# Optimization experiments

Measured on AMD Instinct MI355X. Metric: run time of the kernel, lower is better.

Reference implementation:

```python
import jax, jax.numpy as jnp
import numpy as np

B, S, HID = 2, 2048, 2048
NH, NKV, D = 32, 4, 64
N_REP = NH // NKV
EPS = 1e-6
ROPE_THETA = 10000.0


def _rotate_half(x):
    h = x.shape[-1] // 2
    return jnp.concatenate([-x[..., h:], x[..., :h]], axis=-1)


def _rmsnorm(x, gamma):
    # RMSNorm over last dim (head_dim)
    return x * jax.lax.rsqrt(jnp.mean(x * x, axis=-1, keepdims=True) + EPS) * gamma


def setup_inputs() -> dict:
    key = jax.random.key(0)
    ks = jax.random.split(key, 8)
    hidden_states = jax.random.normal(ks[0], (B, S, HID), dtype=jnp.float32)
    # rotary cos/sin tables, shape [B, S, D]
    pos = jnp.arange(S, dtype=jnp.float32)
    inv_freq = 1.0 / (ROPE_THETA ** (jnp.arange(0, D, 2, dtype=jnp.float32) / D))
    freqs = pos[:, None] * inv_freq[None, :]            # [S, D/2]
    emb = jnp.concatenate([freqs, freqs], axis=-1)      # [S, D]
    cos = jnp.broadcast_to(jnp.cos(emb)[None], (B, S, D))
    sin = jnp.broadcast_to(jnp.sin(emb)[None], (B, S, D))
    sc = 0.02
    Wq = jax.random.normal(ks[1], (NH * D, HID), dtype=jnp.float32) * sc
    Wk = jax.random.normal(ks[2], (NKV * D, HID), dtype=jnp.float32) * sc
    Wv = jax.random.normal(ks[3], (NKV * D, HID), dtype=jnp.float32) * sc
    Wg = jax.random.normal(ks[4], (NH * D, HID), dtype=jnp.float32) * sc
    Wo = jax.random.normal(ks[5], (HID, NH * D), dtype=jnp.float32) * sc
    q_gamma = jnp.ones((D,), dtype=jnp.float32)
    k_gamma = jnp.ones((D,), dtype=jnp.float32)
    return dict(hidden_states=hidden_states, cos=cos, sin=sin,
                Wq=Wq, Wk=Wk, Wv=Wv, Wg=Wg, Wo=Wo,
                q_gamma=q_gamma, k_gamma=k_gamma)


def reference(hidden_states, cos, sin, Wq, Wk, Wv, Wg, Wo, q_gamma, k_gamma):
    b, s, _ = hidden_states.shape
    q = (hidden_states @ Wq.T).reshape(b, s, NH, D)
    k = (hidden_states @ Wk.T).reshape(b, s, NKV, D)
    v = (hidden_states @ Wv.T).reshape(b, s, NKV, D)
    gate = hidden_states @ Wg.T                       # [B, S, NH*D]
    # per-head RMSNorm on q/k
    q = _rmsnorm(q, q_gamma)
    k = _rmsnorm(k, k_gamma)
    # [B, H, S, D]
    q = q.transpose(0, 2, 1, 3)
    k = k.transpose(0, 2, 1, 3)
    v = v.transpose(0, 2, 1, 3)
    # RoPE (unsqueeze_dim=1)
    c = cos[:, None, :, :]
    sn = sin[:, None, :, :]
    q = q * c + _rotate_half(q) * sn
    k = k * c + _rotate_half(k) * sn
    # GQA: repeat kv heads
    kr = jnp.repeat(k, N_REP, axis=1)
    vr = jnp.repeat(v, N_REP, axis=1)
    scaling = D ** -0.5
    scores = jnp.einsum('bhqd,bhkd->bhqk', q, kr) * scaling
    w = jax.nn.softmax(scores.astype(jnp.float32), axis=-1).astype(q.dtype)
    out = jnp.einsum('bhqk,bhkd->bhqd', w, vr)
    out = out.transpose(0, 2, 1, 3).reshape(b, s, NH * D)
    out = out * jax.nn.sigmoid(gate)
    return out @ Wo.T
```

## Files before the change

### kernel.cpp

```cpp
#include <hip/hip_runtime.h>


#define LOG2E 1.44269504088896340736f

typedef __attribute__((ext_vector_type(4))) float f32x4;
typedef __attribute__((ext_vector_type(8))) short bf16x8;

__device__ __forceinline__ float bf2f(unsigned short u) {
  union { unsigned u; float f; } x; x.u = ((unsigned)u) << 16; return x.f;
}
__device__ __forceinline__ unsigned short f2bf(float f) {
  union { float f; unsigned u; } x; x.f = f;
  unsigned r = x.u + 0x7fffu + ((x.u >> 16) & 1u);
  return (unsigned short)(r >> 16);
}

__device__ __forceinline__ void async16(void* lds, const void* g) {
  __builtin_amdgcn_global_load_lds(
      (const __attribute__((address_space(1))) unsigned*)g,
      (__attribute__((address_space(3))) unsigned*)lds, 16, 0, 0);
}
__device__ __forceinline__ void lds_fence() {
  __asm__ volatile("s_waitcnt lgkmcnt(0)" ::: "memory");
}

__global__ __launch_bounds__(256) void cvt_all(
    const float* __restrict__ s0, const float* __restrict__ s1,
    const float* __restrict__ s2, const float* __restrict__ s3,
    const float* __restrict__ s4, const float* __restrict__ s5,
    unsigned short* __restrict__ d0, unsigned short* __restrict__ d1,
    unsigned short* __restrict__ d2, unsigned short* __restrict__ d3,
    unsigned short* __restrict__ d4, unsigned short* __restrict__ d5) {
  const long total = 5505024;
  const long stride = (long)gridDim.x * 256;
  for (long i = (long)blockIdx.x * 256 + threadIdx.x; i < total; i += stride) {
    const float* s; unsigned short* d; long off;
    if      (i < 2097152) { s = s0; d = d0; off = 0; }
    else if (i < 3145728) { s = s1; d = d1; off = 2097152; }
    else if (i < 3276800) { s = s2; d = d2; off = 3145728; }
    else if (i < 3407872) { s = s3; d = d3; off = 3276800; }
    else if (i < 4456448) { s = s4; d = d4; off = 3407872; }
    else                  { s = s5; d = d5; off = 4456448; }
    long j = i - off;
    float4 v = reinterpret_cast<const float4*>(s)[j];
    ushort4 u;
    u.x = f2bf(v.x); u.y = f2bf(v.y); u.z = f2bf(v.z); u.w = f2bf(v.w);
    reinterpret_cast<ushort4*>(d)[j] = u;
  }
}

__device__ __forceinline__ void gemm_main_big(
    const unsigned short* __restrict__ A, const unsigned short* __restrict__ W,
    int m0, int n0, unsigned short* lds, f32x4 acc[4][4]) {
  const int tid = threadIdx.x;
  const int w = tid >> 6, l = tid & 63, quad = l >> 4, l16 = l & 15;
  const int wm = (w & 1) * 64, wn = (w >> 1) * 64;
  const int rlo = tid >> 2, ch = tid & 3;

  const f32x4 Z4 = {0.f, 0.f, 0.f, 0.f};
#pragma unroll
  for (int i = 0; i < 4; i++)
#pragma unroll
    for (int j = 0; j < 4; j++) acc[i][j] = Z4;

  const unsigned short* gA =
      A + (size_t)(m0 + rlo) * 2048 + ((ch ^ ((rlo >> 1) & 3)) * 8);
  const unsigned short* gB =
      W + (size_t)(n0 + rlo) * 2048 + ((ch ^ ((rlo >> 1) & 3)) * 8);

  int arow[4], brow[4];
#pragma unroll
  for (int mt = 0; mt < 4; mt++) arow[mt] = (wm + mt * 16 + l16) * 32;
#pragma unroll
  for (int nt = 0; nt < 4; nt++) brow[nt] = (wn + nt * 16 + l16) * 32;
  const int fx = (quad ^ ((l16 >> 1) & 3)) * 8;

  unsigned short* const bA = lds;
  unsigned short* const bB = lds + 12288;

#pragma unroll
  for (int tt = 0; tt < 2; ++tt) {
    const int ko = tt * 32;
    async16(bA + tt * 4096 + tid * 8,        gA + ko);
    async16(bB + tt * 8192 + tid * 8,        gB + ko);
    async16(bB + tt * 8192 + 4096 + tid * 8, gB + 262144 + ko);
  }
  __asm__ volatile("s_waitcnt vmcnt(3)" ::: "memory");
  __builtin_amdgcn_s_barrier();

  int cb = 0;
  for (int t = 0; t < 64; ++t) {
    unsigned short* cA = bA + cb * 4096;
    unsigned short* cB = bB + cb * 8192;

    if (t < 62) {
      int nb = cb + 2; if (nb >= 3) nb -= 3;
      const int ko = (t + 2) * 32;
      async16(bA + nb * 4096 + tid * 8,        gA + ko);
      async16(bB + nb * 8192 + tid * 8,        gB + ko);
      async16(bB + nb * 8192 + 4096 + tid * 8, gB + 262144 + ko);
    }
    bf16x8 af[4], bf[4];
#pragma unroll
    for (int mt = 0; mt < 4; mt++)
      af[mt] = *(const bf16x8*)&cA[arow[mt] + fx];
#pragma unroll
    for (int nt = 0; nt < 4; nt++)
      bf[nt] = *(const bf16x8*)&cB[brow[nt] + fx];
    __builtin_amdgcn_s_barrier();
    __asm__ volatile("s_waitcnt lgkmcnt(0)" ::: "memory");
    __builtin_amdgcn_sched_barrier(0);
    __builtin_amdgcn_s_setprio(1);
#pragma unroll
    for (int mt = 0; mt < 4; mt++)
#pragma unroll
      for (int nt = 0; nt < 4; nt++)
        acc[mt][nt] = __builtin_amdgcn_mfma_f32_16x16x32_bf16(
            af[mt], bf[nt], acc[mt][nt], 0, 0, 0);
    __builtin_amdgcn_s_setprio(0);
    if (t < 62) {
      __asm__ volatile("s_waitcnt vmcnt(3)" ::: "memory");
    } else if (t == 62) {
      __asm__ volatile("s_waitcnt vmcnt(0)" ::: "memory");
    }
    __builtin_amdgcn_s_barrier();
    cb++; if (cb == 3) cb = 0;
  }
}

__global__ __launch_bounds__(512, 4) void gemm_qkvg(
    const unsigned short* __restrict__ X,
    const unsigned short* __restrict__ Wq, const unsigned short* __restrict__ Wk,
    const unsigned short* __restrict__ Wv, const unsigned short* __restrict__ Wg,
    const float* __restrict__ cosb, const float* __restrict__ sinb,
    const float* __restrict__ qg, const float* __restrict__ kg,
    unsigned short* __restrict__ Qn, unsigned short* __restrict__ Kn,
    unsigned short* __restrict__ Vt, unsigned short* __restrict__ gate) {
  __shared__ __attribute__((aligned(16))) unsigned short lds[36864];
  const int ny = blockIdx.y;
  const unsigned short* W; int n0, type;
  if (ny < 8)       { W = Wq; n0 = ny * 256;        type = 0; }
  else if (ny == 8) { W = Wk; n0 = 0;               type = 1; }
  else if (ny == 9) { W = Wv; n0 = 0;               type = 2; }
  else              { W = Wg; n0 = (ny - 10) * 256; type = 3; }
  const int m0 = blockIdx.x * 128;

  f32x4 acc[4][4];
  gemm_main_big(X, W, m0, n0, lds, acc);

  const int tid = threadIdx.x;
  const int w = tid >> 6, l = tid & 63, quad = l >> 4, l16 = l & 15;
  const int wm = (w & 1) * 64, wn = (w >> 1) * 64;

  if (type == 3) {
#pragma unroll
    for (int mt = 0; mt < 4; mt++)
#pragma unroll
      for (int r = 0; r < 4; r++) {
        int row = m0 + wm + mt * 16 + quad * 4 + r;
#pragma unroll
        for (int nt = 0; nt < 4; nt++)
          gate[(size_t)row * 2048 + n0 + wn + nt * 16 + l16] =
              f2bf(acc[mt][nt][r]);
      }
    return;
  }
  if (type == 2) {
#pragma unroll
    for (int mt = 0; mt < 4; mt++)
#pragma unroll
      for (int r = 0; r < 4; r++) {
        int row = m0 + wm + mt * 16 + quad * 4 + r;
        int b = row >> 11, s = row & 2047;
#pragma unroll
        for (int nt = 0; nt < 4; nt++) {
          int col = wn + nt * 16 + l16;
          int kvh = col >> 6, d = col & 63;
          Vt[((size_t)(b * 4 + kvh) * 64 + d) * 2048 + s] =
              f2bf(acc[mt][nt][r]);
        }
      }
    return;
  }

  const float* gamma = (type == 0) ? qg : kg;
  const float scale  = (type == 0) ? 0.125f : LOG2E;
  const int hb = (n0 + wn) >> 6;
  float gv[4];
#pragma unroll
  for (int nt = 0; nt < 4; nt++) gv[nt] = gamma[nt * 16 + l16];

#pragma unroll
  for (int mt = 0; mt < 4; mt++)
#pragma unroll
    for (int r = 0; r < 4; r++) {
      int row = m0 + wm + mt * 16 + quad * 4 + r;
      float ss = 0.f;
#pragma unroll
      for (int nt = 0; nt < 4; nt++) {
        float v = acc[mt][nt][r]; ss += v * v;
      }
#pragma unroll
      for (int off = 1; off < 16; off <<= 1) ss += __shfl_xor(ss, off);
      float rr = rsqrtf(ss * (1.0f / 64.0f) + 1e-6f);
      float xn[4];
#pragma unroll
      for (int nt = 0; nt < 4; nt++) xn[nt] = acc[mt][nt][r] * rr * gv[nt];
      int b = row >> 11, s = row & 2047;
      unsigned short* dst = (type == 0)
          ? Qn + ((size_t)(b * 32 + hb) * 2048 + s) * 64
          : Kn + ((size_t)(b * 4 + hb) * 2048 + s) * 64;
#pragma unroll
      for (int nt = 0; nt < 4; nt++) {
        int d = nt * 16 + l16;
        float rot = (nt < 2) ? -xn[nt ^ 2] : xn[nt ^ 2];
        float cv = cosb[(size_t)row * 64 + d];
        float sv = sinb[(size_t)row * 64 + d];
        dst[d] = f2bf((xn[nt] * cv + rot * sv) * scale);
      }
    }
}

__global__ __launch_bounds__(512, 2) void gemm_out_k(
    const unsigned short* __restrict__ A, const unsigned short* __restrict__ W,
    float* __restrict__ C) {
  __shared__ __attribute__((aligned(16))) unsigned short lds[65536];
  const int m0 = blockIdx.x * 128, n0 = blockIdx.y * 256;
  f32x4 acc[4][4];
  gemm_main_big(A, W, m0, n0, lds, acc);
  const int tid = threadIdx.x;
  const int w = tid >> 6, l = tid & 63, quad = l >> 4, l16 = l & 15;
  const int wm = (w & 1) * 64, wn = (w >> 1) * 64;
#pragma unroll
  for (int mt = 0; mt < 4; mt++)
#pragma unroll
    for (int nt = 0; nt < 4; nt++) {
      int row = m0 + wm + mt * 16 + quad * 4;
      int col = n0 + wn + nt * 16 + l16;
#pragma unroll
      for (int r = 0; r < 4; r++)
        C[(size_t)(row + r) * 2048 + col] = acc[mt][nt][r];
    }
}

__global__ __launch_bounds__(256, 4) void attn(
    const unsigned short* __restrict__ Qn, const unsigned short* __restrict__ Kn,
    const unsigned short* __restrict__ Vt, const unsigned short* __restrict__ gate,
    unsigned short* __restrict__ act) {
  __shared__ __attribute__((aligned(16))) unsigned short smem[20480];
  unsigned short* Ps = smem + 16384;

  const int tid = threadIdx.x, w = tid >> 6, l = tid & 63;
  const int quad = l >> 4, l16 = l & 15, l7 = l16 & 7;
  const int bh = blockIdx.y, b = bh >> 5, h = bh & 31, kvh = h >> 3;
  const int q0 = blockIdx.x * 128;

  const unsigned short* Qg = Qn + ((size_t)(b * 32 + h) * 2048 + q0) * 64;
  const unsigned short* Kg = Kn + (size_t)(b * 4 + kvh) * 2048 * 64;
  const unsigned short* Vg = Vt + (size_t)(b * 4 + kvh) * 64 * 2048;
  unsigned short* Pw = Ps + w * 1024;

  const int kq_src = ((tid & 7) ^ ((tid >> 3) & 7)) * 8;

#pragma unroll
  for (int i = 0; i < 4; i++)
    async16(smem + i * 2048 + tid * 8,
            Qg + (size_t)(i * 32 + (tid >> 3)) * 64 + kq_src);
  __syncthreads();
  bf16x8 qf[2][2];
#pragma unroll
  for (int mt = 0; mt < 2; mt++)
#pragma unroll
    for (int ks = 0; ks < 2; ks++) {
      int row = w * 32 + mt * 16 + l16;
      qf[mt][ks] = *(const bf16x8*)&smem[row * 64 + ((ks * 4 + quad) ^ l7) * 8];
    }
  __syncthreads();

  const f32x4 Z4 = {0.f, 0.f, 0.f, 0.f};
  f32x4 O[2][4];
  float lp[2][4];
#pragma unroll
  for (int mt = 0; mt < 2; mt++) {
#pragma unroll
    for (int nt = 0; nt < 4; nt++) O[mt][nt] = Z4;
#pragma unroll
    for (int r = 0; r < 4; r++) lp[mt][r] = 0.f;
  }

#pragma unroll
  for (int i = 0; i < 2; i++) {
    async16(smem + i * 2048 + tid * 8,
            Kg + (size_t)(i * 32 + (tid >> 3)) * 64 + kq_src);
    async16(smem + 4096 + i * 2048 + tid * 8,
            Vg + (size_t)(i * 32 + (tid >> 3)) * 2048 + kq_src);
  }

  for (int kt = 0; kt < 32; kt++) {
    __syncthreads();

    if (kt < 31) {
      unsigned short* nb = smem + ((kt + 1) & 1) * 8192;
      const int s1 = (kt + 1) * 64;
#pragma unroll
      for (int i = 0; i < 2; i++) {
        async16(nb + i * 2048 + tid * 8,
                Kg + (size_t)(s1 + i * 32 + (tid >> 3)) * 64 + kq_src);
        async16(nb + 4096 + i * 2048 + tid * 8,
                Vg + (size_t)(i * 32 + (tid >> 3)) * 2048 + s1 + kq_src);
      }
    }

    unsigned short* Ks  = smem + (kt & 1) * 8192;
    unsigned short* Vts = Ks + 4096;

    f32x4 sc[2][4];
#pragma unroll
    for (int mt = 0; mt < 2; mt++)
#pragma unroll
      for (int nt = 0; nt < 4; nt++) sc[mt][nt] = Z4;
    __builtin_amdgcn_s_setprio(1);
#pragma unroll
    for (int nt = 0; nt < 4; nt++) {
      int row = nt * 16 + l16;
      bf16x8 kf0 = *(const bf16x8*)&Ks[row * 64 + (quad ^ l7) * 8];
      bf16x8 kf1 = *(const bf16x8*)&Ks[row * 64 + ((4 + quad) ^ l7) * 8];
#pragma unroll
      for (int mt = 0; mt < 2; mt++) {
        sc[mt][nt] = __builtin_amdgcn_mfma_f32_16x16x32_bf16(qf[mt][0], kf0, sc[mt][nt], 0, 0, 0);
        sc[mt][nt] = __builtin_amdgcn_mfma_f32_16x16x32_bf16(qf[mt][1], kf1, sc[mt][nt], 0, 0, 0);
      }
    }
    __builtin_amdgcn_s_setprio(0);

#pragma unroll
    for (int ks2 = 0; ks2 < 2; ks2++) {
#pragma unroll
      for (int mt = 0; mt < 2; mt++)
#pragma unroll
        for (int ntl = 0; ntl < 2; ntl++) {
          int nt = ks2 * 2 + ntl;
#pragma unroll
          for (int r = 0; r < 4; r++) {
            float p = __builtin_amdgcn_exp2f(sc[mt][nt][r]);
            union { float f; unsigned u; } x; x.f = p;
            union { unsigned u; float f; } t; t.u = x.u & 0xffff0000u;
            lp[mt][r] += t.f;
            int q = mt * 16 + quad * 4 + r;
            int c = ntl * 2 + (l16 >> 3);
            int phys = c ^ ((q >> 1) & 3);
            Pw[q * 32 + phys * 8 + l7] = (unsigned short)(x.u >> 16);
          }
        }
      lds_fence();

      bf16x8 pf[2];
#pragma unroll
      for (int mt = 0; mt < 2; mt++) {
        int q = mt * 16 + l16;
        int phys = quad ^ ((l16 >> 1) & 3);
        pf[mt] = *(const bf16x8*)&Pw[q * 32 + phys * 8];
      }
      __builtin_amdgcn_s_setprio(1);
#pragma unroll
      for (int nt2 = 0; nt2 < 4; nt2++) {
        int d = nt2 * 16 + l16;
        bf16x8 vf = *(const bf16x8*)&Vts[d * 64 + ((ks2 * 4 + quad) ^ l7) * 8];
#pragma unroll
        for (int mt = 0; mt < 2; mt++)
          O[mt][nt2] = __builtin_amdgcn_mfma_f32_16x16x32_bf16(
              pf[mt], vf, O[mt][nt2], 0, 0, 0);
      }
      __builtin_amdgcn_s_setprio(0);
      lds_fence();
    }
  }

#pragma unroll
  for (int mt = 0; mt < 2; mt++)
#pragma unroll
    for (int r = 0; r < 4; r++) {
      float s = lp[mt][r];
#pragma unroll
      for (int off = 1; off < 16; off <<= 1) s += __shfl_xor(s, off);
      lp[mt][r] = s;
    }

#pragma unroll
  for (int mt = 0; mt < 2; mt++) {
    float inv[4];
#pragma unroll
    for (int r = 0; r < 4; r++) inv[r] = 1.0f / lp[mt][r];
#pragma unroll
    for (int nt = 0; nt < 4; nt++)
#pragma unroll
      for (int r = 0; r < 4; r++) {
        int srow = q0 + w * 32 + mt * 16 + quad * 4 + r;
        int col = h * 64 + nt * 16 + l16;
        size_t off = (size_t)(b * 2048 + srow) * 2048 + col;
        float g = bf2f(gate[off]);
        float sig = 1.0f / (1.0f + __builtin_amdgcn_exp2f(-g * LOG2E));
        act[off] = f2bf(O[mt][nt][r] * inv[r] * sig);
      }
  }
}

extern "C" void kernel_launch(void* const* d_in, const int* in_sizes, int n_in,
                              void* d_out, int out_size, void* d_ws, size_t ws_size,
                              hipStream_t stream) {
  const float* hid  = (const float*)d_in[0];
  const float* cosb = (const float*)d_in[1];
  const float* sinb = (const float*)d_in[2];
  const float* Wq   = (const float*)d_in[3];
  const float* Wk   = (const float*)d_in[4];
  const float* Wv   = (const float*)d_in[5];
  const float* Wg   = (const float*)d_in[6];
  const float* Wo   = (const float*)d_in[7];
  const float* qg   = (const float*)d_in[8];
  const float* kg   = (const float*)d_in[9];
  float* out = (float*)d_out;

  char* ws = (char*)d_ws;
  unsigned short* Xb   = (unsigned short*)(ws);
  unsigned short* WqB  = (unsigned short*)(ws + 16777216);
  unsigned short* WkB  = (unsigned short*)(ws + 25165824);
  unsigned short* WvB  = (unsigned short*)(ws + 26214400);
  unsigned short* WgB  = (unsigned short*)(ws + 27262976);
  unsigned short* WoB  = (unsigned short*)(ws + 35651584);
  unsigned short* gate = (unsigned short*)(ws + 44040192);
  unsigned short* Qn   = (unsigned short*)(ws + 60817408);
  unsigned short* Kn   = (unsigned short*)(ws + 77594624);
  unsigned short* Vt   = (unsigned short*)(ws + 79691776);
  unsigned short* act = WqB;

  cvt_all<<<dim3(2048), dim3(256), 0, stream>>>(
      hid, Wq, Wk, Wv, Wg, Wo, Xb, WqB, WkB, WvB, WgB, WoB);

  gemm_qkvg<<<dim3(32, 18), dim3(512), 0, stream>>>(
      Xb, WqB, WkB, WvB, WgB, cosb, sinb, qg, kg, Qn, Kn, Vt, gate);

  attn<<<dim3(16, 64), dim3(256), 0, stream>>>(Qn, Kn, Vt, gate, act);

  gemm_out_k<<<dim3(32, 8), dim3(512), 0, stream>>>(act, WoB, out);
}
```

Measured before the change: 382.7 us.

## Shrink QKVG GEMM tile to 128x128 with 256-thread blocks

Replaces the 128x256-tile, 512-thread QKVG projection GEMM with a 128x128-tile, 256-thread variant that uses a three-stage async LDS pipeline and a smaller shared buffer. The grid doubles to 36 column blocks, and the Vt epilogue now adds the column offset. The aim is more blocks to balance load across CUs and higher occupancy from the reduced LDS footprint. In exchange, each block reuses loaded data less, so global and LDS traffic per FLOP goes up.

```diff
diff --git a/kernel.cpp b/kernel.cpp
--- a/kernel.cpp
+++ b/kernel.cpp
@@ -49,6 +49,87 @@
   }
 }
 
+__device__ __forceinline__ void gemm_core128(
+    const unsigned short* __restrict__ A, const unsigned short* __restrict__ W,
+    int m0, int n0, unsigned short* lds, f32x4 acc[4][4]) {
+  const int tid = threadIdx.x;
+  const int w = tid >> 6, l = tid & 63, quad = l >> 4, l16 = l & 15;
+  const int wm = (w & 1) * 64, wn = (w >> 1) * 64;
+  const int rlo = tid >> 2, ch = tid & 3;
+
+  const f32x4 Z4 = {0.f, 0.f, 0.f, 0.f};
+#pragma unroll
+  for (int i = 0; i < 4; i++)
+#pragma unroll
+    for (int j = 0; j < 4; j++) acc[i][j] = Z4;
+
+  const unsigned short* gA =
+      A + (size_t)(m0 + rlo) * 2048 + ((ch ^ ((rlo >> 1) & 3)) * 8);
+  const unsigned short* gB =
+      W + (size_t)(n0 + rlo) * 2048 + ((ch ^ ((rlo >> 1) & 3)) * 8);
+
+  int arow[4], brow[4];
+#pragma unroll
+  for (int mt = 0; mt < 4; mt++) arow[mt] = (wm + mt * 16 + l16) * 32;
+#pragma unroll
+  for (int nt = 0; nt < 4; nt++) brow[nt] = (wn + nt * 16 + l16) * 32;
+  const int fx = (quad ^ ((l16 >> 1) & 3)) * 8;
+
+  unsigned short* const bA = lds;
+  unsigned short* const bB = lds + 12288;
+
+#pragma unroll
+  for (int tt = 0; tt < 2; ++tt) {
+    const int ko = tt * 32;
+    async16(bA + tt * 4096 + tid * 8,        gA + ko);
+    async16(bA + tt * 4096 + 2048 + tid * 8, gA + 131072 + ko);
+    async16(bB + tt * 4096 + tid * 8,        gB + ko);
+    async16(bB + tt * 4096 + 2048 + tid * 8, gB + 131072 + ko);
+  }
+  __asm__ volatile("s_waitcnt vmcnt(4)" ::: "memory");
+  __builtin_amdgcn_s_barrier();
+
+  int cb = 0;
+  for (int t = 0; t < 64; ++t) {
+    unsigned short* cA = bA + cb * 4096;
+    unsigned short* cB = bB + cb * 4096;
+
+    if (t < 62) {
+      int nb = cb + 2; if (nb >= 3) nb -= 3;
+      const int ko = (t + 2) * 32;
+      async16(bA + nb * 4096 + tid * 8,        gA + ko);
+      async16(bA + nb * 4096 + 2048 + tid * 8, gA + 131072 + ko);
+      async16(bB + nb * 4096 + tid * 8,        gB + ko);
+      async16(bB + nb * 4096 + 2048 + tid * 8, gB + 131072 + ko);
+    }
+    bf16x8 af[4], bf[4];
+#pragma unroll
+    for (int mt = 0; mt < 4; mt++)
+      af[mt] = *(const bf16x8*)&cA[arow[mt] + fx];
+#pragma unroll
+    for (int nt = 0; nt < 4; nt++)
+      bf[nt] = *(const bf16x8*)&cB[brow[nt] + fx];
+    __builtin_amdgcn_s_barrier();
+    __asm__ volatile("s_waitcnt lgkmcnt(0)" ::: "memory");
+    __builtin_amdgcn_sched_barrier(0);
+    __builtin_amdgcn_s_setprio(1);
+#pragma unroll
+    for (int mt = 0; mt < 4; mt++)
+#pragma unroll
+      for (int nt = 0; nt < 4; nt++)
+        acc[mt][nt] = __builtin_amdgcn_mfma_f32_16x16x32_bf16(
+            af[mt], bf[nt], acc[mt][nt], 0, 0, 0);
+    __builtin_amdgcn_s_setprio(0);
+    if (t < 62) {
+      __asm__ volatile("s_waitcnt vmcnt(4)" ::: "memory");
+    } else if (t == 62) {
+      __asm__ volatile("s_waitcnt vmcnt(0)" ::: "memory");
+    }
+    __builtin_amdgcn_s_barrier();
+    cb++; if (cb == 3) cb = 0;
+  }
+}
+
 __device__ __forceinline__ void gemm_main_big(
     const unsigned short* __restrict__ A, const unsigned short* __restrict__ W,
     int m0, int n0, unsigned short* lds, f32x4 acc[4][4]) {
@@ -128,7 +209,7 @@
   }
 }
 
-__global__ __launch_bounds__(512, 4) void gemm_qkvg(
+__global__ __launch_bounds__(256, 3) void gemm_qkvg(
     const unsigned short* __restrict__ X,
     const unsigned short* __restrict__ Wq, const unsigned short* __restrict__ Wk,
     const unsigned short* __restrict__ Wv, const unsigned short* __restrict__ Wg,
@@ -136,17 +217,17 @@
     const float* __restrict__ qg, const float* __restrict__ kg,
     unsigned short* __restrict__ Qn, unsigned short* __restrict__ Kn,
     unsigned short* __restrict__ Vt, unsigned short* __restrict__ gate) {
-  __shared__ __attribute__((aligned(16))) unsigned short lds[36864];
+  __shared__ __attribute__((aligned(16))) unsigned short lds[24576];
   const int ny = blockIdx.y;
   const unsigned short* W; int n0, type;
-  if (ny < 8)       { W = Wq; n0 = ny * 256;        type = 0; }
-  else if (ny == 8) { W = Wk; n0 = 0;               type = 1; }
-  else if (ny == 9) { W = Wv; n0 = 0;               type = 2; }
-  else              { W = Wg; n0 = (ny - 10) * 256; type = 3; }
+  if (ny < 16)      { W = Wq; n0 = ny * 128;        type = 0; }
+  else if (ny < 18) { W = Wk; n0 = (ny - 16) * 128; type = 1; }
+  else if (ny < 20) { W = Wv; n0 = (ny - 18) * 128; type = 2; }
+  else              { W = Wg; n0 = (ny - 20) * 128; type = 3; }
   const int m0 = blockIdx.x * 128;
 
   f32x4 acc[4][4];
-  gemm_main_big(X, W, m0, n0, lds, acc);
+  gemm_core128(X, W, m0, n0, lds, acc);
 
   const int tid = threadIdx.x;
   const int w = tid >> 6, l = tid & 63, quad = l >> 4, l16 = l & 15;
@@ -174,7 +255,7 @@
         int b = row >> 11, s = row & 2047;
 #pragma unroll
         for (int nt = 0; nt < 4; nt++) {
-          int col = wn + nt * 16 + l16;
+          int col = n0 + wn + nt * 16 + l16;
           int kvh = col >> 6, d = col & 63;
           Vt[((size_t)(b * 4 + kvh) * 64 + d) * 2048 + s] =
               f2bf(acc[mt][nt][r]);
@@ -436,7 +517,7 @@
   cvt_all<<<dim3(2048), dim3(256), 0, stream>>>(
       hid, Wq, Wk, Wv, Wg, Wo, Xb, WqB, WkB, WvB, WgB, WoB);
 
-  gemm_qkvg<<<dim3(32, 18), dim3(512), 0, stream>>>(
+  gemm_qkvg<<<dim3(32, 36), dim3(256), 0, stream>>>(
       Xb, WqB, WkB, WvB, WgB, cosb, sinb, qg, kg, Qn, Kn, Vt, gate);
 
   attn<<<dim3(16, 64), dim3(256), 0, stream>>>(Qn, Kn, Vt, gate, act);
```

After: 368.0 us. 1.04x faster.

## Halve GEMM block to 4 waves with 64x128 warp tiles

Applied to the files above, without the earlier changes.

The shared GEMM core now runs 256 threads per block instead of 512. Each wave computes a 64x128 output tile (4x8 MFMA accumulators), and each thread issues twice as many async loads per k-step to fill the same 128x256 block tile. The QK-norm/RoPE epilogue is extended to handle two heads per wave. The aim is more MFMA work per LDS fragment load and fewer waves to synchronize. The cost is higher register pressure, which limits occupancy, and fewer waves to hide latency. gemm_out_k's LDS allocation also shrinks.

```diff
diff --git a/kernel.cpp b/kernel.cpp
--- a/kernel.cpp
+++ b/kernel.cpp
@@ -49,30 +49,30 @@
   }
 }
 
-__device__ __forceinline__ void gemm_main_big(
+__device__ __forceinline__ void gemm_core(
     const unsigned short* __restrict__ A, const unsigned short* __restrict__ W,
-    int m0, int n0, unsigned short* lds, f32x4 acc[4][4]) {
+    int m0, int n0, unsigned short* lds, f32x4 acc[4][8]) {
   const int tid = threadIdx.x;
   const int w = tid >> 6, l = tid & 63, quad = l >> 4, l16 = l & 15;
-  const int wm = (w & 1) * 64, wn = (w >> 1) * 64;
+  const int wm = (w & 1) * 64, wn = (w >> 1) * 128;
   const int rlo = tid >> 2, ch = tid & 3;
 
   const f32x4 Z4 = {0.f, 0.f, 0.f, 0.f};
 #pragma unroll
   for (int i = 0; i < 4; i++)
 #pragma unroll
-    for (int j = 0; j < 4; j++) acc[i][j] = Z4;
+    for (int j = 0; j < 8; j++) acc[i][j] = Z4;
 
   const unsigned short* gA =
       A + (size_t)(m0 + rlo) * 2048 + ((ch ^ ((rlo >> 1) & 3)) * 8);
   const unsigned short* gB =
       W + (size_t)(n0 + rlo) * 2048 + ((ch ^ ((rlo >> 1) & 3)) * 8);
 
-  int arow[4], brow[4];
+  int arow[4], brow[8];
 #pragma unroll
   for (int mt = 0; mt < 4; mt++) arow[mt] = (wm + mt * 16 + l16) * 32;
 #pragma unroll
-  for (int nt = 0; nt < 4; nt++) brow[nt] = (wn + nt * 16 + l16) * 32;
+  for (int nt = 0; nt < 8; nt++) brow[nt] = (wn + nt * 16 + l16) * 32;
   const int fx = (quad ^ ((l16 >> 1) & 3)) * 8;
 
   unsigned short* const bA = lds;
@@ -82,10 +82,13 @@
   for (int tt = 0; tt < 2; ++tt) {
     const int ko = tt * 32;
     async16(bA + tt * 4096 + tid * 8,        gA + ko);
+    async16(bA + tt * 4096 + 2048 + tid * 8, gA + 131072 + ko);
     async16(bB + tt * 8192 + tid * 8,        gB + ko);
+    async16(bB + tt * 8192 + 2048 + tid * 8, gB + 131072 + ko);
     async16(bB + tt * 8192 + 4096 + tid * 8, gB + 262144 + ko);
-  }
-  __asm__ volatile("s_waitcnt vmcnt(3)" ::: "memory");
+    async16(bB + tt * 8192 + 6144 + tid * 8, gB + 393216 + ko);
+  }
+  __asm__ volatile("s_waitcnt vmcnt(6)" ::: "memory");
   __builtin_amdgcn_s_barrier();
 
   int cb = 0;
@@ -97,15 +100,18 @@
       int nb = cb + 2; if (nb >= 3) nb -= 3;
       const int ko = (t + 2) * 32;
       async16(bA + nb * 4096 + tid * 8,        gA + ko);
+      async16(bA + nb * 4096 + 2048 + tid * 8, gA + 131072 + ko);
       async16(bB + nb * 8192 + tid * 8,        gB + ko);
+      async16(bB + nb * 8192 + 2048 + tid * 8, gB + 131072 + ko);
       async16(bB + nb * 8192 + 4096 + tid * 8, gB + 262144 + ko);
-    }
-    bf16x8 af[4], bf[4];
+      async16(bB + nb * 8192 + 6144 + tid * 8, gB + 393216 + ko);
+    }
+    bf16x8 af[4], bf[8];
 #pragma unroll
     for (int mt = 0; mt < 4; mt++)
       af[mt] = *(const bf16x8*)&cA[arow[mt] + fx];
 #pragma unroll
-    for (int nt = 0; nt < 4; nt++)
+    for (int nt = 0; nt < 8; nt++)
       bf[nt] = *(const bf16x8*)&cB[brow[nt] + fx];
     __builtin_amdgcn_s_barrier();
     __asm__ volatile("s_waitcnt lgkmcnt(0)" ::: "memory");
@@ -114,12 +120,12 @@
 #pragma unroll
     for (int mt = 0; mt < 4; mt++)
 #pragma unroll
-      for (int nt = 0; nt < 4; nt++)
+      for (int nt = 0; nt < 8; nt++)
         acc[mt][nt] = __builtin_amdgcn_mfma_f32_16x16x32_bf16(
             af[mt], bf[nt], acc[mt][nt], 0, 0, 0);
     __builtin_amdgcn_s_setprio(0);
     if (t < 62) {
-      __asm__ volatile("s_waitcnt vmcnt(3)" ::: "memory");
+      __asm__ volatile("s_waitcnt vmcnt(6)" ::: "memory");
     } else if (t == 62) {
       __asm__ volatile("s_waitcnt vmcnt(0)" ::: "memory");
     }
@@ -128,7 +134,7 @@
   }
 }
 
-__global__ __launch_bounds__(512, 4) void gemm_qkvg(
+__global__ __launch_bounds__(256, 2) void gemm_qkvg(
     const unsigned short* __restrict__ X,
     const unsigned short* __restrict__ Wq, const unsigned short* __restrict__ Wk,
     const unsigned short* __restrict__ Wv, const unsigned short* __restrict__ Wg,
@@ -145,12 +151,12 @@
   else              { W = Wg; n0 = (ny - 10) * 256; type = 3; }
   const int m0 = blockIdx.x * 128;
 
-  f32x4 acc[4][4];
-  gemm_main_big(X, W, m0, n0, lds, acc);
+  f32x4 acc[4][8];
+  gemm_core(X, W, m0, n0, lds, acc);
 
   const int tid = threadIdx.x;
   const int w = tid >> 6, l = tid & 63, quad = l >> 4, l16 = l & 15;
-  const int wm = (w & 1) * 64, wn = (w >> 1) * 64;
+  const int wm = (w & 1) * 64, wn = (w >> 1) * 128;
 
   if (type == 3) {
 #pragma unroll
@@ -159,7 +165,7 @@
       for (int r = 0; r < 4; r++) {
         int row = m0 + wm + mt * 16 + quad * 4 + r;
 #pragma unroll
-        for (int nt = 0; nt < 4; nt++)
+        for (int nt = 0; nt < 8; nt++)
           gate[(size_t)row * 2048 + n0 + wn + nt * 16 + l16] =
               f2bf(acc[mt][nt][r]);
       }
@@ -173,7 +179,7 @@
         int row = m0 + wm + mt * 16 + quad * 4 + r;
         int b = row >> 11, s = row & 2047;
 #pragma unroll
-        for (int nt = 0; nt < 4; nt++) {
+        for (int nt = 0; nt < 8; nt++) {
           int col = wn + nt * 16 + l16;
           int kvh = col >> 6, d = col & 63;
           Vt[((size_t)(b * 4 + kvh) * 64 + d) * 2048 + s] =
@@ -185,56 +191,69 @@
 
   const float* gamma = (type == 0) ? qg : kg;
   const float scale  = (type == 0) ? 0.125f : LOG2E;
-  const int hb = (n0 + wn) >> 6;
-  float gv[4];
-#pragma unroll
-  for (int nt = 0; nt < 4; nt++) gv[nt] = gamma[nt * 16 + l16];
+  const int hb0 = (n0 + wn) >> 6;
+  float gv[8];
+#pragma unroll
+  for (int nt = 0; nt < 8; nt++) gv[nt] = gamma[(nt & 3) * 16 + l16];
 
 #pragma unroll
   for (int mt = 0; mt < 4; mt++)
 #pragma unroll
     for (int r = 0; r < 4; r++) {
       int row = m0 + wm + mt * 16 + quad * 4 + r;
-      float ss = 0.f;
+      float ss0 = 0.f, ss1 = 0.f;
 #pragma unroll
       for (int nt = 0; nt < 4; nt++) {
-        float v = acc[mt][nt][r]; ss += v * v;
-      }
-#pragma unroll
-      for (int off = 1; off < 16; off <<= 1) ss += __shfl_xor(ss, off);
-      float rr = rsqrtf(ss * (1.0f / 64.0f) + 1e-6f);
-      float xn[4];
-#pragma unroll
-      for (int nt = 0; nt < 4; nt++) xn[nt] = acc[mt][nt][r] * rr * gv[nt];
+        float v = acc[mt][nt][r]; ss0 += v * v;
+      }
+#pragma unroll
+      for (int nt = 4; nt < 8; nt++) {
+        float v = acc[mt][nt][r]; ss1 += v * v;
+      }
+#pragma unroll
+      for (int off = 1; off < 16; off <<= 1) {
+        ss0 += __shfl_xor(ss0, off);
+        ss1 += __shfl_xor(ss1, off);
+      }
+      float rr0 = rsqrtf(ss0 * (1.0f / 64.0f) + 1e-6f);
+      float rr1 = rsqrtf(ss1 * (1.0f / 64.0f) + 1e-6f);
+      float xn[8];
+#pragma unroll
+      for (int nt = 0; nt < 8; nt++)
+        xn[nt] = acc[mt][nt][r] * ((nt < 4) ? rr0 : rr1) * gv[nt];
       int b = row >> 11, s = row & 2047;
-      unsigned short* dst = (type == 0)
-          ? Qn + ((size_t)(b * 32 + hb) * 2048 + s) * 64
-          : Kn + ((size_t)(b * 4 + hb) * 2048 + s) * 64;
-#pragma unroll
-      for (int nt = 0; nt < 4; nt++) {
-        int d = nt * 16 + l16;
-        float rot = (nt < 2) ? -xn[nt ^ 2] : xn[nt ^ 2];
+      unsigned short* dst0 = (type == 0)
+          ? Qn + ((size_t)(b * 32 + hb0) * 2048 + s) * 64
+          : Kn + ((size_t)(b * 4 + hb0) * 2048 + s) * 64;
+      unsigned short* dst1 = (type == 0)
+          ? Qn + ((size_t)(b * 32 + hb0 + 1) * 2048 + s) * 64
+          : Kn + ((size_t)(b * 4 + hb0 + 1) * 2048 + s) * 64;
+#pragma unroll
+      for (int nt = 0; nt < 8; nt++) {
+        int d = (nt & 3) * 16 + l16;
+        float rot = ((nt & 3) < 2) ? -xn[nt ^ 2] : xn[nt ^ 2];
         float cv = cosb[(size_t)row * 64 + d];
         float sv = sinb[(size_t)row * 64 + d];
-        dst[d] = f2bf((xn[nt] * cv + rot * sv) * scale);
-      }
-    }
-}
-
-__global__ __launch_bounds__(512, 2) void gemm_out_k(
+        float val = (xn[nt] * cv + rot * sv) * scale;
+        ((nt < 4) ? dst0 : dst1)[d] = f2bf(val);
+      }
+    }
+}
+
+__global__ __launch_bounds__(256, 2) void gemm_out_k(
     const unsigned short* __restrict__ A, const unsigned short* __restrict__ W,
     float* __restrict__ C) {
-  __shared__ __attribute__((aligned(16))) unsigned short lds[65536];
+  __shared__ __attribute__((aligned(16))) unsigned short lds[36864];
   const int m0 = blockIdx.x * 128, n0 = blockIdx.y * 256;
-  f32x4 acc[4][4];
-  gemm_main_big(A, W, m0, n0, lds, acc);
+  f32x4 acc[4][8];
+  gemm_core(A, W, m0, n0, lds, acc);
   const int tid = threadIdx.x;
   const int w = tid >> 6, l = tid & 63, quad = l >> 4, l16 = l & 15;
-  const int wm = (w & 1) * 64, wn = (w >> 1) * 64;
+  const int wm = (w & 1) * 64, wn = (w >> 1) * 128;
 #pragma unroll
   for (int mt = 0; mt < 4; mt++)
 #pragma unroll
-    for (int nt = 0; nt < 4; nt++) {
+    for (int nt = 0; nt < 8; nt++) {
       int row = m0 + wm + mt * 16 + quad * 4;
       int col = n0 + wn + nt * 16 + l16;
 #pragma unroll
@@ -436,10 +455,10 @@
   cvt_all<<<dim3(2048), dim3(256), 0, stream>>>(
       hid, Wq, Wk, Wv, Wg, Wo, Xb, WqB, WkB, WvB, WgB, WoB);
 
-  gemm_qkvg<<<dim3(32, 18), dim3(512), 0, stream>>>(
+  gemm_qkvg<<<dim3(32, 18), dim3(256), 0, stream>>>(
       Xb, WqB, WkB, WvB, WgB, cosb, sinb, qg, kg, Qn, Kn, Vt, gate);
 
   attn<<<dim3(16, 64), dim3(256), 0, stream>>>(Qn, Kn, Vt, gate, act);
 
-  gemm_out_k<<<dim3(32, 8), dim3(512), 0, stream>>>(act, WoB, out);
-}
+  gemm_out_k<<<dim3(32, 8), dim3(256), 0, stream>>>(act, WoB, out);
+}
```

After: 391.5 us. 1.02x slower.
